# Optimization experiments

Hardware: AMD Instinct MI355X
Metric: run time of the kernel (lower is better)

The kernel has to match this reference:

```python
import jax, jax.numpy as jnp
import numpy as np

B, T, U = 4, 256, 100
H_ENC, H_DEC = 512, 512
INPUT_SIZE = H_ENC + H_DEC  # 1024, joint='concat'
INNER = 512
VOCAB = 1024


def setup_inputs() -> dict:
    key = jax.random.key(0)
    k1, k2, k3, k4, k5, k6 = jax.random.split(key, 6)
    s_in = 1.0 / np.sqrt(INPUT_SIZE)
    s_h = 1.0 / np.sqrt(INNER)
    return {
        "enc_state": jax.random.normal(k1, (B, T, H_ENC), dtype=jnp.float32),
        "dec_state": jax.random.normal(k2, (B, U, H_DEC), dtype=jnp.float32),
        # mlp[0]: Linear(input_size -> inner): W1 [inner, input_size], b1 [inner]
        "W1": jax.random.uniform(k3, (INNER, INPUT_SIZE), jnp.float32, -s_in, s_in),
        "b1": jax.random.uniform(k4, (INNER,), jnp.float32, -s_in, s_in),
        # mlp[2]: Linear(inner -> vocab): W2 [vocab, inner], b2 [vocab]
        "W2": jax.random.uniform(k5, (VOCAB, INNER), jnp.float32, -s_h, s_h),
        "b2": jax.random.uniform(k6, (VOCAB,), jnp.float32, -s_h, s_h),
    }


def reference(enc_state, dec_state, W1, b1, W2, b2):
    # joint='concat': concat([enc broadcast over U, dec broadcast over T], -1)
    # then Linear -> tanh -> Linear.
    # Mathematically identical fused form: split W1 into enc/dec column blocks,
    # project each at native size, broadcast-add.
    h_enc = H_ENC
    W1e = W1[:, :h_enc]   # [inner, H_enc]
    W1d = W1[:, h_enc:]   # [inner, H_dec]
    pe = jnp.einsum('bth,ih->bti', enc_state, W1e)  # [B,T,inner]
    pd = jnp.einsum('buh,ih->bui', dec_state, W1d)  # [B,U,inner]
    hidden = jnp.tanh(pe[:, :, None, :] + pd[:, None, :, :] + b1)  # [B,T,U,inner]
    joint = jnp.einsum('btui,vi->btuv', hidden, W2) + b2  # [B,T,U,vocab]
    return joint
```

## Files before the change

### kernel.cpp

```cpp
#include <hip/hip_runtime.h>
#include <hip/hip_bf16.h>

#define NB 4
#define NT 256
#define NU 100
#define NH 512
#define NI 512
#define NV 1024
#define MROWS (NB * NT * NU)

typedef __attribute__((ext_vector_type(16))) float f32x16;
typedef __attribute__((ext_vector_type(8))) __bf16 bf16x8;

static __device__ __forceinline__ unsigned int f2bf(float f) {
  unsigned int u = __float_as_uint(f);
  return (u + 0x7FFFu + ((u >> 16) & 1u)) >> 16;
}

static __device__ __forceinline__ float fast_tanh(float x) {
  float e = __expf(2.f * x);
  return 1.f - 2.f * __builtin_amdgcn_rcpf(1.f + e);
}

static __device__ __forceinline__ unsigned int cvt_pk_bf16(float lo, float hi) {
  unsigned int r;
  asm("v_cvt_pk_bf16_f32 %0, %1, %2" : "=v"(r) : "v"(lo), "v"(hi));
  return r;
}

__global__ __launch_bounds__(256) void prep_kernel(
    const float* __restrict__ enc, const float* __restrict__ dec,
    const float* __restrict__ W1, const float* __restrict__ W2,
    float* __restrict__ pe, float* __restrict__ pd,
    unsigned short* __restrict__ w2g) {
  const int bx = blockIdx.x;
  const int tx = threadIdx.x;
  if (bx >= 23) {
    int c = ((bx - 23) * 8 + blockIdx.y) * 256 + tx;
    int lane = c & 63, ntl = (c >> 6) & 7, ks = (c >> 9) & 31, np = c >> 14;
    int col = np * 256 + ntl * 32 + (lane & 31);
    int k = ks * 16 + (lane >> 5) * 8;
    const float* src = W2 + (size_t)col * NI + k;
    float4 a = *(const float4*)src;
    float4 b = *(const float4*)(src + 4);
    uint4 o;
    o.x = f2bf(a.x) | (f2bf(a.y) << 16);
    o.y = f2bf(a.z) | (f2bf(a.w) << 16);
    o.z = f2bf(b.x) | (f2bf(b.y) << 16);
    o.w = f2bf(b.z) | (f2bf(b.w) << 16);
    *(uint4*)(w2g + (size_t)c * 8) = o;
    return;
  }
  __shared__ float As[64][17];
  __shared__ float Bs[64][17];
  const float* A;
  float* P;
  int Mrows, colOff, row0;
  if (bx < 16) { A = enc; P = pe; Mrows = NB * NT; colOff = 0;  row0 = bx * 64; }
  else         { A = dec; P = pd; Mrows = NB * NU; colOff = NH; row0 = (bx - 16) * 64; }
  const int col0 = blockIdx.y * 64;
  const int tr = tx >> 4, tc = tx & 15;
  const int lr = tx >> 2, lc = (tx & 3) * 4;
  float acc[4][4] = {};
  for (int k0 = 0; k0 < NH; k0 += 16) {
    float4 av = make_float4(0.f, 0.f, 0.f, 0.f);
    if (row0 + lr < Mrows)
      av = *(const float4*)(A + (size_t)(row0 + lr) * NH + k0 + lc);
    float4 bv = *(const float4*)(W1 + (size_t)(col0 + lr) * (NH + NH) + colOff + k0 + lc);
    As[lr][lc] = av.x; As[lr][lc + 1] = av.y; As[lr][lc + 2] = av.z; As[lr][lc + 3] = av.w;
    Bs[lr][lc] = bv.x; Bs[lr][lc + 1] = bv.y; Bs[lr][lc + 2] = bv.z; Bs[lr][lc + 3] = bv.w;
    __syncthreads();
#pragma unroll
    for (int kk = 0; kk < 16; ++kk) {
      float a4[4], b4[4];
#pragma unroll
      for (int i = 0; i < 4; ++i) { a4[i] = As[tr * 4 + i][kk]; b4[i] = Bs[tc * 4 + i][kk]; }
#pragma unroll
      for (int i = 0; i < 4; ++i)
#pragma unroll
        for (int j = 0; j < 4; ++j) acc[i][j] = fmaf(a4[i], b4[j], acc[i][j]);
    }
    __syncthreads();
  }
#pragma unroll
  for (int i = 0; i < 4; ++i) {
    int r = row0 + tr * 4 + i;
    if (r < Mrows) {
#pragma unroll
      for (int j = 0; j < 4; ++j)
        P[(size_t)r * NI + col0 + tc * 4 + j] = acc[i][j];
    }
  }
}

__global__ __launch_bounds__(512, 4) void fused_joint_kernel(
    const float* __restrict__ pe, const float* __restrict__ pd,
    const float* __restrict__ b1, const unsigned short* __restrict__ w2g,
    const float* __restrict__ b2, float* __restrict__ out) {
  __shared__ unsigned char ldsA[65536];
  const int tx = threadIdx.x;
  const int R0 = blockIdx.x * 64;
  const int lane = tx & 63, wid = tx >> 6;
  const int wr = wid >> 2, wc = wid & 3;
  const int l31 = lane & 31, lh = lane >> 5;

  const unsigned char* w2p = (const unsigned char*)w2g;
  const unsigned char* bBase0 = w2p + ((wc * 2 + 0) * 64 + lane) * 16;
  const unsigned char* bBase1 = w2p + ((wc * 2 + 1) * 64 + lane) * 16;

#define LOADB(SET, G) do {                                                    \
    SET##0 = *(const bf16x8*)(bBase0 + ((size_t)(G) << 13));                  \
    SET##1 = *(const bf16x8*)(bBase1 + ((size_t)(G) << 13));                  \
  } while (0)

  bf16x8 s00, s01, s10, s11, s20, s21, s30, s31;
  LOADB(s0, 0); LOADB(s1, 1); LOADB(s2, 2); LOADB(s3, 3);

#pragma unroll 2
  for (int pass = 0; pass < 8; ++pass) {
    int idx = pass * 512 + tx;
    int row = idx >> 6;
    int g8 = idx & 63;
    int i0 = g8 * 8;
    int grow = R0 + row;
    int b = grow / (NT * NU);
    int rem = grow - b * (NT * NU);
    int t = rem / NU;
    int u = rem - t * NU;
    const float* peP = pe + (size_t)(b * NT + t) * NI + i0;
    const float* pdP = pd + (size_t)(b * NU + u) * NI + i0;
    float4 p0 = *(const float4*)peP, p1 = *(const float4*)(peP + 4);
    float4 q0 = *(const float4*)pdP, q1 = *(const float4*)(pdP + 4);
    float4 c0 = *(const float4*)(b1 + i0), c1 = *(const float4*)(b1 + i0 + 4);
    uint4 pk;
    pk.x = cvt_pk_bf16(fast_tanh(p0.x + q0.x + c0.x), fast_tanh(p0.y + q0.y + c0.y));
    pk.y = cvt_pk_bf16(fast_tanh(p0.z + q0.z + c0.z), fast_tanh(p0.w + q0.w + c0.w));
    pk.z = cvt_pk_bf16(fast_tanh(p1.x + q1.x + c1.x), fast_tanh(p1.y + q1.y + c1.y));
    pk.w = cvt_pk_bf16(fast_tanh(p1.z + q1.z + c1.z), fast_tanh(p1.w + q1.w + c1.w));
    *(uint4*)(ldsA + row * 1024 + ((g8 ^ (row & 7)) << 4)) = pk;
  }
  __syncthreads();

  f32x16 acc0, acc1;
#pragma unroll
  for (int z = 0; z < 16; ++z) { acc0[z] = 0.f; acc1[z] = 0.f; }

  const int aRowBase = (wr * 32 + l31) * 1024;
  const int rx = l31 & 7;

#define STEP(SET, G) do {                                                     \
    const int ks_ = (G) & 31;                                                 \
    bf16x8 af_ = *(const bf16x8*)(ldsA + aRowBase +                           \
                                  (((ks_ * 2 + lh) ^ rx) << 4));              \
    __builtin_amdgcn_s_setprio(1);                                            \
    acc0 = __builtin_amdgcn_mfma_f32_32x32x16_bf16(af_, SET##0, acc0, 0, 0, 0); \
    acc1 = __builtin_amdgcn_mfma_f32_32x32x16_bf16(af_, SET##1, acc1, 0, 0, 0); \
    __builtin_amdgcn_s_setprio(0);                                            \
    if (ks_ == 31) {                                                          \
      const int np_ = (G) >> 5;                                               \
      int c0_ = np_ * 256 + wc * 64 + l31;                                    \
      float bb0_ = b2[c0_];                                                   \
      float bb1_ = b2[c0_ + 32];                                              \
      _Pragma("unroll")                                                       \
      for (int r_ = 0; r_ < 16; ++r_) {                                       \
        int grow_ = R0 + wr * 32 + (r_ & 3) + 8 * (r_ >> 2) + 4 * lh;         \
        float* op_ = out + (size_t)grow_ * NV + c0_;                          \
        op_[0]  = acc0[r_] + bb0_;                                            \
        op_[32] = acc1[r_] + bb1_;                                            \
        acc0[r_] = 0.f;                                                       \
        acc1[r_] = 0.f;                                                       \
      }                                                                       \
    }                                                                         \
  } while (0)

  for (int g = 0; g < 128; g += 4) {
    STEP(s0, g);     if (g + 4 < 128) LOADB(s0, g + 4);
    STEP(s1, g + 1); if (g + 5 < 128) LOADB(s1, g + 5);
    STEP(s2, g + 2); if (g + 6 < 128) LOADB(s2, g + 6);
    STEP(s3, g + 3); if (g + 7 < 128) LOADB(s3, g + 7);
  }
#undef STEP
#undef LOADB
}

extern "C" void kernel_launch(void* const* d_in, const int* in_sizes, int n_in,
                              void* d_out, int out_size, void* d_ws, size_t ws_size,
                              hipStream_t stream) {
  const float* enc = (const float*)d_in[0];
  const float* dec = (const float*)d_in[1];
  const float* W1  = (const float*)d_in[2];
  const float* b1  = (const float*)d_in[3];
  const float* W2  = (const float*)d_in[4];
  const float* b2  = (const float*)d_in[5];
  float* out = (float*)d_out;
  char* ws = (char*)d_ws;

  float* pe = (float*)ws;
  float* pd = (float*)(ws + (2u << 20));
  unsigned short* w2g = (unsigned short*)(ws + (3u << 20));

  prep_kernel<<<dim3(55, 8), 256, 0, stream>>>(enc, dec, W1, W2, pe, pd, w2g);
  fused_joint_kernel<<<MROWS / 64, 512, 0, stream>>>(pe, pd, b1, w2g, b2, out);
}
```

Before: 259.0 us.

## Enlarge joint GEMM row tile to 128 with each wave covering all rows

Each block now processes 128 rows of the joint hidden matrix instead of 64, using 128KB of LDS. Each wave owns one 32-column slice of W2 and all four 32-row sub-tiles, so every W2 fragment loaded from global memory feeds four MFMAs instead of two. This halves W2 global traffic per output. The cost is double LDS and more accumulator registers, which lowers occupancy to 2 blocks per CU, and half as many blocks.

```diff
diff --git a/kernel.cpp b/kernel.cpp
--- a/kernel.cpp
+++ b/kernel.cpp
@@ -93,31 +93,28 @@
   }
 }
 
-__global__ __launch_bounds__(512, 4) void fused_joint_kernel(
+__global__ __launch_bounds__(512, 2) void fused_joint_kernel(
     const float* __restrict__ pe, const float* __restrict__ pd,
     const float* __restrict__ b1, const unsigned short* __restrict__ w2g,
     const float* __restrict__ b2, float* __restrict__ out) {
-  __shared__ unsigned char ldsA[65536];
+  __shared__ unsigned char ldsA[131072];
   const int tx = threadIdx.x;
-  const int R0 = blockIdx.x * 64;
+  const int R0 = blockIdx.x * 128;
   const int lane = tx & 63, wid = tx >> 6;
-  const int wr = wid >> 2, wc = wid & 3;
   const int l31 = lane & 31, lh = lane >> 5;
 
   const unsigned char* w2p = (const unsigned char*)w2g;
-  const unsigned char* bBase0 = w2p + ((wc * 2 + 0) * 64 + lane) * 16;
-  const unsigned char* bBase1 = w2p + ((wc * 2 + 1) * 64 + lane) * 16;
+  const unsigned char* bBase = w2p + ((size_t)(wid * 64 + lane)) * 16;
 
 #define LOADB(SET, G) do {                                                    \
-    SET##0 = *(const bf16x8*)(bBase0 + ((size_t)(G) << 13));                  \
-    SET##1 = *(const bf16x8*)(bBase1 + ((size_t)(G) << 13));                  \
+    SET = *(const bf16x8*)(bBase + ((size_t)(G) << 13));                      \
   } while (0)
 
-  bf16x8 s00, s01, s10, s11, s20, s21, s30, s31;
+  bf16x8 s0, s1, s2, s3;
   LOADB(s0, 0); LOADB(s1, 1); LOADB(s2, 2); LOADB(s3, 3);
 
 #pragma unroll 2
-  for (int pass = 0; pass < 8; ++pass) {
+  for (int pass = 0; pass < 16; ++pass) {
     int idx = pass * 512 + tx;
     int row = idx >> 6;
     int g8 = idx & 63;
@@ -141,34 +138,40 @@
   }
   __syncthreads();
 
-  f32x16 acc0, acc1;
-#pragma unroll
-  for (int z = 0; z < 16; ++z) { acc0[z] = 0.f; acc1[z] = 0.f; }
-
-  const int aRowBase = (wr * 32 + l31) * 1024;
+  f32x16 acc[4];
+#pragma unroll
+  for (int m = 0; m < 4; ++m)
+#pragma unroll
+    for (int z = 0; z < 16; ++z) acc[m][z] = 0.f;
+
+  const int aBase = l31 * 1024;
   const int rx = l31 & 7;
 
 #define STEP(SET, G) do {                                                     \
     const int ks_ = (G) & 31;                                                 \
-    bf16x8 af_ = *(const bf16x8*)(ldsA + aRowBase +                           \
-                                  (((ks_ * 2 + lh) ^ rx) << 4));              \
+    const int so_ = (((ks_ * 2 + lh) ^ rx) << 4);                             \
+    bf16x8 af0_ = *(const bf16x8*)(ldsA + aBase + so_);                       \
+    bf16x8 af1_ = *(const bf16x8*)(ldsA + aBase + 32768 + so_);               \
+    bf16x8 af2_ = *(const bf16x8*)(ldsA + aBase + 65536 + so_);               \
+    bf16x8 af3_ = *(const bf16x8*)(ldsA + aBase + 98304 + so_);               \
     __builtin_amdgcn_s_setprio(1);                                            \
-    acc0 = __builtin_amdgcn_mfma_f32_32x32x16_bf16(af_, SET##0, acc0, 0, 0, 0); \
-    acc1 = __builtin_amdgcn_mfma_f32_32x32x16_bf16(af_, SET##1, acc1, 0, 0, 0); \
+    acc[0] = __builtin_amdgcn_mfma_f32_32x32x16_bf16(af0_, SET, acc[0], 0, 0, 0); \
+    acc[1] = __builtin_amdgcn_mfma_f32_32x32x16_bf16(af1_, SET, acc[1], 0, 0, 0); \
+    acc[2] = __builtin_amdgcn_mfma_f32_32x32x16_bf16(af2_, SET, acc[2], 0, 0, 0); \
+    acc[3] = __builtin_amdgcn_mfma_f32_32x32x16_bf16(af3_, SET, acc[3], 0, 0, 0); \
     __builtin_amdgcn_s_setprio(0);                                            \
     if (ks_ == 31) {                                                          \
       const int np_ = (G) >> 5;                                               \
-      int c0_ = np_ * 256 + wc * 64 + l31;                                    \
-      float bb0_ = b2[c0_];                                                   \
-      float bb1_ = b2[c0_ + 32];                                              \
+      int col_ = np_ * 256 + wid * 32 + l31;                                  \
+      float bb_ = b2[col_];                                                   \
       _Pragma("unroll")                                                       \
-      for (int r_ = 0; r_ < 16; ++r_) {                                       \
-        int grow_ = R0 + wr * 32 + (r_ & 3) + 8 * (r_ >> 2) + 4 * lh;         \
-        float* op_ = out + (size_t)grow_ * NV + c0_;                          \
-        op_[0]  = acc0[r_] + bb0_;                                            \
-        op_[32] = acc1[r_] + bb1_;                                            \
-        acc0[r_] = 0.f;                                                       \
-        acc1[r_] = 0.f;                                                       \
+      for (int m_ = 0; m_ < 4; ++m_) {                                        \
+        _Pragma("unroll")                                                     \
+        for (int r_ = 0; r_ < 16; ++r_) {                                     \
+          int grow_ = R0 + m_ * 32 + (r_ & 3) + 8 * (r_ >> 2) + 4 * lh;       \
+          out[(size_t)grow_ * NV + col_] = acc[m_][r_] + bb_;                 \
+          acc[m_][r_] = 0.f;                                                  \
+        }                                                                     \
       }                                                                       \
     }                                                                         \
   } while (0)
@@ -200,5 +203,5 @@
   unsigned short* w2g = (unsigned short*)(ws + (3u << 20));
 
   prep_kernel<<<dim3(55, 8), 256, 0, stream>>>(enc, dec, W1, W2, pe, pd, w2g);
-  fused_joint_kernel<<<MROWS / 64, 512, 0, stream>>>(pe, pd, b1, w2g, b2, out);
-}
+  fused_joint_kernel<<<MROWS / 128, 512, 0, stream>>>(pe, pd, b1, w2g, b2, out);
+}
```

Result: slower. 414.8 us (+60.1%).
